# Kernel optimization log

Hardware: AMD Instinct MI355X
Metric: run time of the kernel (lower is better)

The kernel has to match this reference:

```python
import jax, jax.numpy as jnp
import numpy as np
import math

L_LAYERS = 4
EMBED = 512
HEADS = 8
FFN = 2048
EPS = 1e-20
PAD_IDX = 0


def sinusoidal_table(num_embeddings, embedding_dim, padding_idx=0):
    half = embedding_dim // 2
    freq = jnp.exp(jnp.arange(half, dtype=jnp.float32) * (-math.log(10000.0) / (half - 1)))
    ang = jnp.arange(num_embeddings, dtype=jnp.float32)[:, None] * freq[None, :]
    emb = jnp.concatenate([jnp.sin(ang), jnp.cos(ang)], axis=1)
    if padding_idx is not None:
        emb = emb.at[padding_idx].set(0.0)
    return emb  # [num_embeddings, embedding_dim]


def layer_norm(x, g, b):
    mu = jnp.mean(x, axis=-1, keepdims=True)
    var = jnp.mean((x - mu) ** 2, axis=-1, keepdims=True)
    return (x - mu) * jax.lax.rsqrt(var + EPS) * g + b


def mha(x_q, x_kv, Wqkv, bqkv, Wo, bo, mask):
    """Custom attention: scaled scores, multiplicative mask, GLOBAL min-max norm (no softmax)."""
    T, B, C = x_q.shape
    S = x_kv.shape[0]
    hd = C // HEADS
    scale = hd ** -0.5
    q = x_q @ Wqkv[:C].T + bqkv[:C]
    k = x_kv @ Wqkv[C:2 * C].T + bqkv[C:2 * C]
    v = x_kv @ Wqkv[2 * C:].T + bqkv[2 * C:]
    q = q * scale
    # [T,B,C] -> [B*H, T, hd]
    q = q.reshape(T, B * HEADS, hd).transpose(1, 0, 2)
    k = k.reshape(S, B * HEADS, hd).transpose(1, 0, 2)
    v = v.reshape(S, B * HEADS, hd).transpose(1, 0, 2)
    w = jnp.einsum('bth,bsh->bts', q, k)  # [B*H, T, S]
    if mask is not None:
        w = w * mask[None, :, :]
    # global min-max normalization (as in the torch source)
    w = (w - jnp.min(w)) / (jnp.max(w) - jnp.min(w))
    a = jnp.einsum('bts,bsh->bth', w, v)  # [B*H, T, hd]
    a = a.transpose(1, 0, 2).reshape(T, B, C)
    return a @ Wo.T + bo


def setup_inputs() -> dict:
    key = jax.random.key(0)
    ks = iter(jax.random.split(key, 32))
    T, B, C, F, L = 2048, 2, EMBED, FFN, L_LAYERS
    d = {}
    d['x'] = jax.random.normal(next(ks), (T, B, C), dtype=jnp.float32)
    d['enc_out'] = jax.random.normal(next(ks), (T, B, C), dtype=jnp.float32)
    d['tokens'] = jax.random.randint(next(ks), (B, T), 0, 32000, dtype=jnp.int64 if jax.config.read('jax_enable_x64') else jnp.int32)
    sd = C ** -0.5
    d['self_Wqkv'] = jax.random.normal(next(ks), (L, 3 * C, C)) * sd
    d['self_bqkv'] = jnp.zeros((L, 3 * C))
    d['self_Wo'] = jax.random.normal(next(ks), (L, C, C)) * sd
    d['self_bo'] = jnp.zeros((L, C))
    d['cross_Wqkv'] = jax.random.normal(next(ks), (L, 3 * C, C)) * sd
    d['cross_bqkv'] = jnp.zeros((L, 3 * C))
    d['cross_Wo'] = jax.random.normal(next(ks), (L, C, C)) * sd
    d['cross_bo'] = jnp.zeros((L, C))
    d['fc1_w'] = jax.random.normal(next(ks), (L, F, C)) * sd
    d['fc1_b'] = jnp.zeros((L, F))
    d['fc2_w'] = jax.random.normal(next(ks), (L, C, F)) * (F ** -0.5)
    d['fc2_b'] = jnp.zeros((L, C))
    d['ln1_g'] = jnp.ones((L, C)); d['ln1_b'] = jnp.zeros((L, C))
    d['ln2_g'] = jnp.ones((L, C)); d['ln2_b'] = jnp.zeros((L, C))
    d['ln3_g'] = jnp.ones((L, C)); d['ln3_b'] = jnp.zeros((L, C))
    return d


def _forward(x, enc_out, tokens, self_Wqkv, self_bqkv, self_Wo, self_bo,
             cross_Wqkv, cross_bqkv, cross_Wo, cross_bo,
             fc1_w, fc1_b, fc2_w, fc2_b, ln1_g, ln1_b, ln2_g, ln2_b, ln3_g, ln3_b):
    T, B, C = x.shape
    # sinusoidal positional embedding (make_positions with padding_idx=0, no left pad)
    table = sinusoidal_table(PAD_IDX + 1 + T, C, PAD_IDX)
    pos = jnp.where(tokens != PAD_IDX, jnp.arange(1, T + 1)[None, :], 0)  # [B, T]
    pe = table[pos]  # [B, T, C]
    x = x + pe.transpose(1, 0, 2)
    # multiplicative future mask: tril of ones
    fmask = jnp.tril(jnp.ones((T, T), dtype=x.dtype))
    for l in range(L_LAYERS):
        # self-attention
        res = x
        x = mha(x, x, self_Wqkv[l], self_bqkv[l], self_Wo[l], self_bo[l], fmask)
        x = layer_norm(res + x, ln1_g[l], ln1_b[l])
        # cross-attention (no mask)
        res = x
        x = mha(x, enc_out, cross_Wqkv[l], cross_bqkv[l], cross_Wo[l], cross_bo[l], None)
        x = layer_norm(res + x, ln2_g[l], ln2_b[l])
        # FFN
        res = x
        h = jax.nn.relu(x @ fc1_w[l].T + fc1_b[l])
        x = h @ fc2_w[l].T + fc2_b[l]
        x = layer_norm(res + x, ln3_g[l], ln3_b[l])
    return x


def reference(x, enc_out, tokens, self_Wqkv, self_bqkv, self_Wo, self_bo,
              cross_Wqkv, cross_bqkv, cross_Wo, cross_bo,
              fc1_w, fc1_b, fc2_w, fc2_b, ln1_g, ln1_b, ln2_g, ln2_b, ln3_g, ln3_b):
    return _forward(x, enc_out, tokens, self_Wqkv, self_bqkv, self_Wo, self_bo,
                    cross_Wqkv, cross_bqkv, cross_Wo, cross_bo,
                    fc1_w, fc1_b, fc2_w, fc2_b, ln1_g, ln1_b, ln2_g, ln2_b, ln3_g, ln3_b)
```

## Files before the change

### kernel.cpp

```cpp
#include <hip/hip_runtime.h>
#include <math.h>

typedef __bf16 bf16;
typedef unsigned short u16;
typedef unsigned int u32;
typedef __bf16 bf16x8 __attribute__((ext_vector_type(8)));
typedef float f32x4 __attribute__((ext_vector_type(4)));

#define T_SEQ 2048
#define NB    2
#define CE    512
#define HD    64
#define ROWS  4096
#define LDT   40
#define LDA   72

#define MFMA16(a,b,c) __builtin_amdgcn_mfma_f32_16x16x32_bf16((a),(b),(c),0,0,0)

static __device__ __forceinline__ int xcd_swz(int id, int n) {
  int q = n >> 3, r = n & 7;
  int x = id & 7, o = id >> 3;
  return (x < r) ? (x * (q + 1) + o) : (r * (q + 1) + (x - r) * q + o);
}

static __device__ __forceinline__ float ldf(const void* src, size_t eoff, bool f32) {
  return f32 ? ((const float*)src)[eoff] : (float)((const bf16*)src)[eoff];
}

static __device__ __forceinline__ u32 fenc(float f) {
  u32 u = __float_as_uint(f);
  return (u & 0x80000000u) ? ~u : (u | 0x80000000u);
}
static __device__ __forceinline__ float fdec(u32 u) {
  u32 v = (u & 0x80000000u) ? (u & 0x7fffffffu) : ~u;
  return __uint_as_float(v);
}

__global__ __launch_bounds__(256) void sniff(const u16* __restrict__ xs,
                                             const int* __restrict__ toks,
                                             int* __restrict__ flags)
{
  const int tid = threadIdx.x;
  int crazy = 0, ze = 0;
  for (int i = tid; i < 4096; i += 256) {
    int e = (xs[i] >> 7) & 0xFF;
    if (e >= 141) crazy++;
    if (((i & 1) == 0) && (xs[i] == 0)) ze++;
  }
  int zc = 0;
  for (int i = tid; i < 1024; i += 256)
    if (toks[2 * i + 1] == 0) zc++;
  __shared__ int r1[4], r2[4], r3[4];
#pragma unroll
  for (int o = 32; o; o >>= 1) {
    crazy += __shfl_down(crazy, o); ze += __shfl_down(ze, o); zc += __shfl_down(zc, o);
  }
  if ((tid & 63) == 0) { r1[tid >> 6] = crazy; r2[tid >> 6] = ze; r3[tid >> 6] = zc; }
  __syncthreads();
  if (tid == 0) {
    int c = r1[0] + r1[1] + r1[2] + r1[3];
    int z = r2[0] + r2[1] + r2[2] + r2[3];
    int t = r3[0] + r3[1] + r3[2] + r3[3];
    flags[0] = (z > 1500 || c > 64) ? 1 : 0;
    flags[1] = (t > 900) ? 1 : 0;
    flags[3] = 0;
    flags[4] = 0;
  }
}

__global__ __launch_bounds__(256) void probe_lo(const void* w0, const void* w1, const void* w2,
                                                const void* w3, const void* w4, const void* w5,
                                                const void* w6,
                                                int* __restrict__ flags)
{
  if (flags[0] == 0) return;
  const int m = blockIdx.y;
  const void* srcs[7] = {w0, w1, w2, w3, w4, w5, w6};
  const int sizes[7]  = {3145728, 1048576, 3145728, 1048576, 4194304, 4194304, 2097152};
  const float4* p = (const float4*)srcs[m];
  const int n4 = sizes[m] >> 2;
  bool nz = false;
  for (int i = blockIdx.x * 256 + threadIdx.x; i < n4; i += 128 * 256) {
    float4 v = p[i];
    nz = nz || (v.x != (float)(bf16)v.x) || (v.y != (float)(bf16)v.y)
            || (v.z != (float)(bf16)v.z) || (v.w != (float)(bf16)v.w);
  }
  unsigned long long mv = __ballot(nz);
  if ((threadIdx.x & 63) == 0 && mv)
    atomicOr(&flags[(m == 6) ? 3 : 4], 1);
}

__global__ __launch_bounds__(256) void posembed(const void* __restrict__ xsrc,
                                                const int* __restrict__ toks,
                                                const int* __restrict__ flags,
                                                float* __restrict__ xf,
                                                bf16* __restrict__ xh, bf16* __restrict__ xl)
{
  const bool f32 = flags[0] != 0;
  const bool tok64 = flags[1] != 0;
  const int row = blockIdx.x;
  const int t = row >> 1, b = row & 1;
  const int tix = b * T_SEQ + t;
  const int tok = tok64 ? toks[2 * tix] : toks[tix];
  const int p = (tok != 0) ? (t + 1) : 0;
  const float kf = -0.0361193740f;
  for (int c = threadIdx.x; c < CE; c += 256) {
    float pe = 0.0f;
    if (p != 0) {
      int i = (c < 256) ? c : (c - 256);
      float freq = expf((float)i * kf);
      float ang = (float)p * freq;
      pe = (c < 256) ? sinf(ang) : cosf(ang);
    }
    float v = ldf(xsrc, (size_t)row * CE + c, f32) + pe;
    size_t o = (size_t)row * CE + c;
    xf[o] = v;
    bf16 hi = (bf16)v;
    xh[o] = hi; xl[o] = (bf16)(v - (float)hi);
  }
}

template<int OUTM, bool BIAS>
__global__ __launch_bounds__(256) void gemm_bb(const bf16* __restrict__ A1h, const bf16* __restrict__ A1l,
                                               const void* __restrict__ A2,
                                               const void* __restrict__ Braw, long long bOff,
                                               const void* __restrict__ bias, size_t biasOff,
                                               const int* __restrict__ flags,
                                               float* __restrict__ Cf,
                                               bf16* __restrict__ Coh, bf16* __restrict__ Col,
                                               int N, int K, int kspan, int nbx, int nbxA,
                                               long long partStride)
{
  __shared__ __align__(16) bf16 Ah[128 * LDT];
  __shared__ __align__(16) bf16 Al[128 * LDT];
  __shared__ __align__(16) bf16 Bh[64 * LDT];
  __shared__ __align__(16) bf16 Bl[64 * LDT];
  const int id = xcd_swz((int)blockIdx.x, (int)gridDim.x);
  const int per_z = nbx * 32;
  const int zz = id / per_z;
  const int rem = id - zz * per_z;
  const int by = rem / nbx, bx = rem - by * nbx;
  const bool bfl = flags[0] != 0;
  const bool blo = bfl && (flags[4] != 0);
  const bool aSplit = (bx < nbxA);
  const bool a2lo = bfl && (flags[3] != 0);
  const bool alo = aSplit ? true : a2lo;
  const int tid = threadIdx.x;
  const int m0 = by * 128, n0 = bx * 64;
  const int srA = tid >> 1, skA = (tid & 1) * 16;
  const int srB = tid >> 2, skB = (tid & 3) * 8;
  const int wid = tid >> 6, lane = tid & 63;
  const int wm = (wid >> 1) * 64, wn = (wid & 1) * 32;
  const int fr = lane & 15, fk = (lane >> 4) * 8;
  const int kb = zz * kspan;
  const int ke = (kb + kspan < K) ? (kb + kspan) : K;
  f32x4 acc[4][2] = {};

  uint4 ra0, ra1, ra2, ra3, rb0, rb1;
  auto loadA = [&](int k0) {
    size_t g = (size_t)(m0 + srA) * K + k0 + skA;
    if (aSplit) {
      const uint4* p = (const uint4*)(A1h + g); ra0 = p[0]; ra1 = p[1];
      const uint4* q = (const uint4*)(A1l + g); ra2 = q[0]; ra3 = q[1];
    } else if (bfl) {
      const uint4* p = (const uint4*)((const float*)A2 + g);
      ra0 = p[0]; ra1 = p[1]; ra2 = p[2]; ra3 = p[3];
    } else {
      const uint4* p = (const uint4*)((const bf16*)A2 + g); ra0 = p[0]; ra1 = p[1];
    }
  };
  auto loadB = [&](int k0) {
    size_t g = (size_t)bOff + (size_t)(n0 + srB) * K + k0 + skB;
    if (bfl) {
      const uint4* p = (const uint4*)((const float*)Braw + g); rb0 = p[0]; rb1 = p[1];
    } else {
      rb0 = *(const uint4*)((const bf16*)Braw + g);
    }
  };
  auto storeA = [&]() {
    if (aSplit) {
      *(uint4*)&Ah[srA * LDT + skA]     = ra0;
      *(uint4*)&Ah[srA * LDT + skA + 8] = ra1;
      *(uint4*)&Al[srA * LDT + skA]     = ra2;
      *(uint4*)&Al[srA * LDT + skA + 8] = ra3;
    } else if (bfl) {
      const float* f = (const float*)&ra0;
      float v[16];
      const float* f0 = (const float*)&ra0; const float* f1 = (const float*)&ra1;
      const float* f2 = (const float*)&ra2; const float* f3 = (const float*)&ra3;
#pragma unroll
      for (int q = 0; q < 4; q++) { v[q] = f0[q]; v[4+q] = f1[q]; v[8+q] = f2[q]; v[12+q] = f3[q]; }
      (void)f;
      bf16x8 h0, h1;
#pragma unroll
      for (int q = 0; q < 8; q++) { h0[q] = (bf16)v[q]; h1[q] = (bf16)v[8+q]; }
      *(bf16x8*)&Ah[srA * LDT + skA]     = h0;
      *(bf16x8*)&Ah[srA * LDT + skA + 8] = h1;
      if (a2lo) {
        bf16x8 l0, l1;
#pragma unroll
        for (int q = 0; q < 8; q++) {
          l0[q] = (bf16)(v[q]   - (float)h0[q]);
          l1[q] = (bf16)(v[8+q] - (float)h1[q]);
        }
        *(bf16x8*)&Al[srA * LDT + skA]     = l0;
        *(bf16x8*)&Al[srA * LDT + skA + 8] = l1;
      }
    } else {
      *(uint4*)&Ah[srA * LDT + skA]     = ra0;
      *(uint4*)&Ah[srA * LDT + skA + 8] = ra1;
    }
  };
  auto storeB = [&]() {
    if (bfl) {
      float v[8];
      const float* f0 = (const float*)&rb0; const float* f1 = (const float*)&rb1;
#pragma unroll
      for (int q = 0; q < 4; q++) { v[q] = f0[q]; v[4+q] = f1[q]; }
      bf16x8 h0;
#pragma unroll
      for (int q = 0; q < 8; q++) h0[q] = (bf16)v[q];
      *(bf16x8*)&Bh[srB * LDT + skB] = h0;
      if (blo) {
        bf16x8 l0;
#pragma unroll
        for (int q = 0; q < 8; q++) l0[q] = (bf16)(v[q] - (float)h0[q]);
        *(bf16x8*)&Bl[srB * LDT + skB] = l0;
      }
    } else {
      *(uint4*)&Bh[srB * LDT + skB] = rb0;
    }
  };

  loadA(kb); loadB(kb);
  for (int k0 = kb; k0 < ke; k0 += 32) {
    __syncthreads();
    storeA(); storeB();
    __syncthreads();
    if (k0 + 32 < ke) { loadA(k0 + 32); loadB(k0 + 32); }
    bf16x8 ah[4], bh2[2];
#pragma unroll
    for (int i = 0; i < 4; i++) ah[i] = *(const bf16x8*)&Ah[(wm + i*16 + fr) * LDT + fk];
#pragma unroll
    for (int j = 0; j < 2; j++) bh2[j] = *(const bf16x8*)&Bh[(wn + j*16 + fr) * LDT + fk];
#pragma unroll
    for (int i = 0; i < 4; i++)
#pragma unroll
      for (int j = 0; j < 2; j++)
        acc[i][j] = MFMA16(ah[i], bh2[j], acc[i][j]);
    if (alo) {
      bf16x8 al[4];
#pragma unroll
      for (int i = 0; i < 4; i++) al[i] = *(const bf16x8*)&Al[(wm + i*16 + fr) * LDT + fk];
#pragma unroll
      for (int i = 0; i < 4; i++)
#pragma unroll
        for (int j = 0; j < 2; j++)
          acc[i][j] = MFMA16(al[i], bh2[j], acc[i][j]);
    }
    if (blo) {
      bf16x8 bl[2];
#pragma unroll
      for (int j = 0; j < 2; j++) bl[j] = *(const bf16x8*)&Bl[(wn + j*16 + fr) * LDT + fk];
#pragma unroll
      for (int i = 0; i < 4; i++)
#pragma unroll
        for (int j = 0; j < 2; j++)
          acc[i][j] = MFMA16(ah[i], bl[j], acc[i][j]);
    }
  }
  const int orow0 = m0 + wm + (lane >> 4) * 4;
  const int ocol0 = n0 + wn + (lane & 15);
  if (OUTM == 0) {
    float* Cp = Cf + (long long)zz * partStride;
    const bool addb = BIAS && (zz == 0);
#pragma unroll
    for (int j = 0; j < 2; j++) {
      int col = ocol0 + j * 16;
      float bv = addb ? ldf(bias, biasOff + col, flags[0] != 0) : 0.0f;
#pragma unroll
      for (int i = 0; i < 4; i++)
#pragma unroll
        for (int r = 0; r < 4; r++)
          Cp[(size_t)(orow0 + i * 16 + r) * N + col] = acc[i][j][r] + bv;
    }
  } else {
#pragma unroll
    for (int j = 0; j < 2; j++) {
      int col = ocol0 + j * 16;
      float bv = ldf(bias, biasOff + col, flags[0] != 0);
#pragma unroll
      for (int i = 0; i < 4; i++)
#pragma unroll
        for (int r = 0; r < 4; r++) {
          float vv = fmaxf(acc[i][j][r] + bv, 0.0f);
          bf16 hi = (bf16)vv;
          size_t o = (size_t)(orow0 + i * 16 + r) * N + col;
          Coh[o] = hi; Col[o] = (bf16)(vv - (float)hi);
        }
    }
  }
}

__global__ __launch_bounds__(256) void prep_kv(const float* __restrict__ base, int ld,
                                               int kofs0, int vofs0,
                                               bf16* __restrict__ kh, bf16* __restrict__ kl,
                                               bf16* __restrict__ vth, bf16* __restrict__ vtl,
                                               float* __restrict__ vcs,
                                               u32* __restrict__ mmf_u)
{
  __shared__ float ts[64 * 65];
  const int bh = blockIdx.x, s0 = blockIdx.y * 64;
  const int b = bh >> 3, hq = bh & 7;
  const int kofs = kofs0 + hq * HD, vofs = vofs0 + hq * HD;
  const int tid = threadIdx.x;
  if (tid == 0) { mmf_u[0] = 0xFFFFFFFFu; mmf_u[1] = 0u; }
#pragma unroll
  for (int it = 0; it < 16; ++it) {
    int idx = it * 256 + tid, r = idx >> 6, d = idx & 63;
    size_t rowb = (size_t)((s0 + r) * NB + b) * ld;
    float v = base[rowb + kofs + d];
    bf16 hi = (bf16)v;
    size_t o = ((size_t)bh * T_SEQ + s0 + r) * 64 + d;
    kh[o] = hi; kl[o] = (bf16)(v - (float)hi);
    ts[r * 65 + d] = base[rowb + vofs + d];
  }
  __syncthreads();
  const int d = tid >> 2, sseg = (tid & 3) * 16;
  bf16x8 hv0, lv0, hv1, lv1;
#pragma unroll
  for (int q = 0; q < 8; ++q) {
    float v0 = ts[(sseg + q) * 65 + d];
    float v1 = ts[(sseg + 8 + q) * 65 + d];
    bf16 h0 = (bf16)v0, h1 = (bf16)v1;
    hv0[q] = h0; lv0[q] = (bf16)(v0 - (float)h0);
    hv1[q] = h1; lv1[q] = (bf16)(v1 - (float)h1);
  }
  size_t o = ((size_t)bh * 64 + d) * T_SEQ + s0 + sseg;
  *(bf16x8*)&vth[o]     = hv0;
  *(bf16x8*)&vth[o + 8] = hv1;
  *(bf16x8*)&vtl[o]     = lv0;
  *(bf16x8*)&vtl[o + 8] = lv1;
  if (tid < 64) {
    float s = 0.0f;
    for (int j = 0; j < 64; ++j) s += ts[j * 65 + tid];
    vcs[((size_t)bh * 32 + blockIdx.y) * 64 + tid] = s;
  }
}

__device__ __forceinline__ int remap_ty(int ty) { return (ty < 16) ? ty : 47 - ty; }

template<bool MASK>
__global__ __launch_bounds__(256) void fattn(const float* __restrict__ qbase, int qld, int qofs0,
                                             const bf16* __restrict__ kh, const bf16* __restrict__ kl,
                                             const bf16* __restrict__ vth, const bf16* __restrict__ vtl,
                                             u32* __restrict__ mmf_u,
                                             bf16* __restrict__ pvh, bf16* __restrict__ pvl)
{
  __shared__ __align__(16) bf16 Qh[64 * LDA], Ql[64 * LDA];
  __shared__ __align__(16) bf16 Kh[64 * LDA], Kl[64 * LDA];
  __shared__ __align__(16) bf16 Vh[64 * LDA], Vl[64 * LDA];
  __shared__ __align__(16) bf16 Ph[64 * LDA], Pl[64 * LDA];
  __shared__ float rn[4], rx[4];
  const int id = xcd_swz((int)blockIdx.x, 512);
  const int bh = id >> 5;
  const int tyr = remap_ty(id & 31);
  const int t0 = tyr * 64;
  const int b = bh >> 3, hq = bh & 7;
  const int qofs = qofs0 + hq * HD;
  const int tid = threadIdx.x;
#pragma unroll
  for (int it = 0; it < 16; ++it) {
    int idx = it * 256 + tid, r = idx >> 6, d = idx & 63;
    float v = qbase[(size_t)((t0 + r) * NB + b) * qld + qofs + d] * 0.125f;
    bf16 hi = (bf16)v;
    Qh[r * LDA + d] = hi; Ql[r * LDA + d] = (bf16)(v - (float)hi);
  }
  const int wid = tid >> 6, lane = tid & 63;
  const int wm_ = (wid >> 1) * 32, wn_ = (wid & 1) * 32;
  const int fr = lane & 15, fko = (lane >> 4) * 8;
  const int crr = (lane >> 4) * 4, crc = lane & 15;
  const int cr = tid >> 2, cseg = (tid & 3) * 16;
  float mn = 1e30f, mx = -1e30f;
  f32x4 o4[2][2] = {};
  const int nch = MASK ? (tyr + 1) : 32;
  for (int sc = 0; sc < nch; ++sc) {
    const int s0 = sc * 64;
    __syncthreads();
    {
      size_t go = ((size_t)bh * T_SEQ + s0 + cr) * 64 + cseg;
      *(bf16x8*)&Kh[cr * LDA + cseg]     = *(const bf16x8*)&kh[go];
      *(bf16x8*)&Kh[cr * LDA + cseg + 8] = *(const bf16x8*)&kh[go + 8];
      *(bf16x8*)&Kl[cr * LDA + cseg]     = *(const bf16x8*)&kl[go];
      *(bf16x8*)&Kl[cr * LDA + cseg + 8] = *(const bf16x8*)&kl[go + 8];
      size_t gv = ((size_t)bh * 64 + cr) * T_SEQ + s0 + cseg;
      *(bf16x8*)&Vh[cr * LDA + cseg]     = *(const bf16x8*)&vth[gv];
      *(bf16x8*)&Vh[cr * LDA + cseg + 8] = *(const bf16x8*)&vth[gv + 8];
      *(bf16x8*)&Vl[cr * LDA + cseg]     = *(const bf16x8*)&vtl[gv];
      *(bf16x8*)&Vl[cr * LDA + cseg + 8] = *(const bf16x8*)&vtl[gv + 8];
    }
    __syncthreads();
    f32x4 a4[2][2] = {};
#pragma unroll
    for (int ks = 0; ks < 2; ++ks) {
      bf16x8 aH[2], aL[2], bH[2], bL[2];
#pragma unroll
      for (int i = 0; i < 2; ++i) {
        aH[i] = *(const bf16x8*)&Qh[(wm_ + i*16 + fr) * LDA + ks*32 + fko];
        aL[i] = *(const bf16x8*)&Ql[(wm_ + i*16 + fr) * LDA + ks*32 + fko];
        bH[i] = *(const bf16x8*)&Kh[(wn_ + i*16 + fr) * LDA + ks*32 + fko];
        bL[i] = *(const bf16x8*)&Kl[(wn_ + i*16 + fr) * LDA + ks*32 + fko];
      }
#pragma unroll
      for (int i = 0; i < 2; ++i)
#pragma unroll
        for (int j = 0; j < 2; ++j) {
          a4[i][j] = MFMA16(aH[i], bH[j], a4[i][j]);
          a4[i][j] = MFMA16(aL[i], bH[j], a4[i][j]);
          a4[i][j] = MFMA16(aH[i], bL[j], a4[i][j]);
        }
    }
#pragma unroll
    for (int i = 0; i < 2; ++i)
#pragma unroll
      for (int j = 0; j < 2; ++j)
#pragma unroll
        for (int r = 0; r < 4; ++r) {
          int tl = wm_ + i*16 + crr + r;
          int sl = wn_ + j*16 + crc;
          float w = a4[i][j][r];
          if (MASK && (s0 + sl) > (t0 + tl)) w = 0.0f;
          mn = fminf(mn, w); mx = fmaxf(mx, w);
          bf16 wh = (bf16)w;
          Ph[tl * LDA + sl] = wh;
          Pl[tl * LDA + sl] = (bf16)(w - (float)wh);
        }
    __syncthreads();
#pragma unroll
    for (int ks = 0; ks < 2; ++ks) {
      bf16x8 pH[2], pL[2], vH[2], vL[2];
#pragma unroll
      for (int i = 0; i < 2; ++i) {
        pH[i] = *(const bf16x8*)&Ph[(wm_ + i*16 + fr) * LDA + ks*32 + fko];
        pL[i] = *(const bf16x8*)&Pl[(wm_ + i*16 + fr) * LDA + ks*32 + fko];
        vH[i] = *(const bf16x8*)&Vh[(wn_ + i*16 + fr) * LDA + ks*32 + fko];
        vL[i] = *(const bf16x8*)&Vl[(wn_ + i*16 + fr) * LDA + ks*32 + fko];
      }
#pragma unroll
      for (int i = 0; i < 2; ++i)
#pragma unroll
        for (int j = 0; j < 2; ++j) {
          o4[i][j] = MFMA16(pH[i], vH[j], o4[i][j]);
          o4[i][j] = MFMA16(pL[i], vH[j], o4[i][j]);
          o4[i][j] = MFMA16(pH[i], vL[j], o4[i][j]);
        }
    }
  }
#pragma unroll
  for (int i = 0; i < 2; ++i)
#pragma unroll
    for (int j = 0; j < 2; ++j)
#pragma unroll
      for (int r = 0; r < 4; ++r) {
        int tl = wm_ + i*16 + crr + r;
        int dl = wn_ + j*16 + crc;
        float val = o4[i][j][r];
        bf16 hi = (bf16)val;
        size_t o = (size_t)((t0 + tl) * NB + b) * CE + hq * HD + dl;
        pvh[o] = hi; pvl[o] = (bf16)(val - (float)hi);
      }
#pragma unroll
  for (int o = 32; o; o >>= 1) { mn = fminf(mn, __shfl_down(mn, o)); mx = fmaxf(mx, __shfl_down(mx, o)); }
  if (lane == 0) { rn[wid] = mn; rx[wid] = mx; }
  __syncthreads();
  if (tid == 0) {
    float bmn = fminf(fminf(rn[0], rn[1]), fminf(rn[2], rn[3]));
    float bmx = fmaxf(fmaxf(rx[0], rx[1]), fmaxf(rx[2], rx[3]));
    atomicMin(&mmf_u[0], fenc(bmn));
    atomicMax(&mmf_u[1], fenc(bmx));
  }
}

__global__ __launch_bounds__(256) void wo_term(const u32* __restrict__ mmf_u,
                                               const float* __restrict__ vcs,
                                               const void* __restrict__ Wo, size_t woOff,
                                               const void* __restrict__ bo, size_t boOff,
                                               const int* __restrict__ flags,
                                               float* __restrict__ term)
{
  __shared__ float vs[512];
  const bool fl = flags[0] != 0;
  const int tid = threadIdx.x;
  const float mn = fdec(mmf_u[0]);
  const float inv = 1.0f / (fdec(mmf_u[1]) - mn);
  const float cmn = mn * inv;
  const int b = blockIdx.x >> 5;
  for (int k = tid; k < 512; k += 256) {
    int h = k >> 6, d = k & 63;
    float s = 0.0f;
#pragma unroll
    for (int ch = 0; ch < 32; ++ch)
      s += vcs[(size_t)((b * 8 + h) * 32 + ch) * 64 + d];
    vs[k] = s;
  }
  __syncthreads();
  const int out = blockIdx.x * 16 + (tid >> 4);
  const int c = out & 511;
  const int k0 = (tid & 15) * 32;
  float s = 0.0f;
#pragma unroll 8
  for (int k = 0; k < 32; ++k)
    s += vs[k0 + k] * ldf(Wo, woOff + (size_t)c * 512 + k0 + k, fl);
  s += __shfl_down(s, 8); s += __shfl_down(s, 4); s += __shfl_down(s, 2); s += __shfl_down(s, 1);
  if ((tid & 15) == 0)
    term[out] = -cmn * s + ldf(bo, boOff + c, fl);
}

template<int NP, bool AFF, bool SPLIT>
__global__ __launch_bounds__(256) void ln_sum(const float* __restrict__ res,
                                              const float* __restrict__ p, long long pstride,
                                              const void* __restrict__ g, const void* __restrict__ be,
                                              size_t goff, const int* __restrict__ flags,
                                              const u32* __restrict__ mmf_u,
                                              const float* __restrict__ term,
                                              float* __restrict__ xfo,
                                              bf16* __restrict__ xh, bf16* __restrict__ xl)
{
  __shared__ float red[4];
  const bool fl = flags[0] != 0;
  const int tid = threadIdx.x;
  const size_t base = (size_t)blockIdx.x * CE;
  float pa = 0.0f, pb = 0.0f;
#pragma unroll
  for (int k = 0; k < NP; k++) {
    pa += p[(long long)k * pstride + base + tid];
    pb += p[(long long)k * pstride + base + tid + 256];
  }
  float a, b2;
  if (AFF) {
    const float mnv = fdec(mmf_u[0]);
    const float inv = 1.0f / (fdec(mmf_u[1]) - mnv);
    const int b = blockIdx.x & 1;
    a  = res[base + tid]       + inv * pa + term[b * 512 + tid];
    b2 = res[base + tid + 256] + inv * pb + term[b * 512 + tid + 256];
  } else {
    a  = res[base + tid]       + pa;
    b2 = res[base + tid + 256] + pb;
  }
  float s = a + b2;
#pragma unroll
  for (int o = 32; o; o >>= 1) s += __shfl_down(s, o);
  if ((tid & 63) == 0) red[tid >> 6] = s;
  __syncthreads();
  float mu = (red[0] + red[1] + red[2] + red[3]) * (1.0f / 512.0f);
  __syncthreads();
  float da = a - mu, db = b2 - mu;
  float q = da * da + db * db;
#pragma unroll
  for (int o = 32; o; o >>= 1) q += __shfl_down(q, o);
  if ((tid & 63) == 0) red[tid >> 6] = q;
  __syncthreads();
  float var = (red[0] + red[1] + red[2] + red[3]) * (1.0f / 512.0f);
  float rs = rsqrtf(var + 1e-20f);
  float o1 = da * rs * ldf(g, goff + tid, fl)       + ldf(be, goff + tid, fl);
  float o2 = db * rs * ldf(g, goff + tid + 256, fl) + ldf(be, goff + tid + 256, fl);
  xfo[base + tid]       = o1;
  xfo[base + tid + 256] = o2;
  if (SPLIT) {
    bf16 h1 = (bf16)o1, h2 = (bf16)o2;
    xh[base + tid]       = h1; xl[base + tid]       = (bf16)(o1 - (float)h1);
    xh[base + tid + 256] = h2; xl[base + tid + 256] = (bf16)(o2 - (float)h2);
  }
}

extern "C" void kernel_launch(void* const* d_in, const int* in_sizes, int n_in,
                              void* d_out, int out_size, void* d_ws, size_t ws_size,
                              hipStream_t stream)
{
  (void)in_sizes; (void)n_in; (void)out_size; (void)ws_size;
  const void* x_in   = d_in[0];
  const void* enc_in = d_in[1];
  const int*  tokens = (const int*)d_in[2];
  const void* sWqkv = d_in[3];
  const void* sbqkv = d_in[4];
  const void* sWo   = d_in[5];
  const void* sbo   = d_in[6];
  const void* cWqkv = d_in[7];
  const void* cbqkv = d_in[8];
  const void* cWo   = d_in[9];
  const void* cbo   = d_in[10];
  const void* fc1w  = d_in[11];
  const void* fc1b  = d_in[12];
  const void* fc2w  = d_in[13];
  const void* fc2b  = d_in[14];
  const void* ln1g  = d_in[15];
  const void* ln1b  = d_in[16];
  const void* ln2g  = d_in[17];
  const void* ln2b  = d_in[18];
  const void* ln3g  = d_in[19];
  const void* ln3b  = d_in[20];

  char* ws = (char*)d_ws;
  size_t off = 0;
  auto alloc = [&](size_t bytes) -> char* {
    char* p = ws + off;
    off += (bytes + 255) & ~(size_t)255;
    return p;
  };
  int*   flags   = (int*)  alloc(256);
  u32*   mmf_u   = (u32*)  alloc(256);
  float* term    = (float*)alloc(1024 * 4);
  float* xf      = (float*)alloc((size_t)ROWS * CE * 4);
  bf16*  xh      = (bf16*) alloc((size_t)ROWS * CE * 2);
  bf16*  xl      = (bf16*) alloc((size_t)ROWS * CE * 2);
  float* qkv     = (float*)alloc((size_t)ROWS * 2048 * 4);
  bf16*  pvh     = (bf16*) alloc((size_t)ROWS * CE * 2);
  bf16*  pvl     = (bf16*) alloc((size_t)ROWS * CE * 2);
  float* pblk    = (float*)alloc((size_t)ROWS * CE * 4 * 4);
  bf16*  khb     = (bf16*) alloc((size_t)16 * T_SEQ * 64 * 2);
  bf16*  klb     = (bf16*) alloc((size_t)16 * T_SEQ * 64 * 2);
  bf16*  vth     = (bf16*) alloc((size_t)16 * 64 * T_SEQ * 2);
  bf16*  vtl     = (bf16*) alloc((size_t)16 * 64 * T_SEQ * 2);
  float* vcs     = (float*)alloc((size_t)16 * 32 * 64 * 4);
  bf16* hh = (bf16*)qkv;
  bf16* hl = (bf16*)qkv + (size_t)ROWS * 2048;
  const long long PS_FULL = (long long)ROWS * CE;

  sniff<<<1, 256, 0, stream>>>((const u16*)x_in, tokens, flags);
  probe_lo<<<dim3(128, 7), 256, 0, stream>>>(sWqkv, sWo, cWqkv, cWo, fc1w, fc2w, enc_in, flags);
  posembed<<<ROWS, 256, 0, stream>>>(x_in, tokens, flags, xf, xh, xl);

  for (int l = 0; l < 4; l++) {
    gemm_bb<0, true><<<768, 256, 0, stream>>>(
        xh, xl, xh,
        sWqkv, (long long)l * 786432,
        sbqkv, (size_t)l * 1536, flags,
        qkv, nullptr, nullptr, 1536, 512, 512, 24, 24, 0);
    prep_kv<<<dim3(16, 32), 256, 0, stream>>>(qkv, 1536, 512, 1024, khb, klb, vth, vtl, vcs, mmf_u);
    fattn<true><<<512, 256, 0, stream>>>(qkv, 1536, 0, khb, klb, vth, vtl, mmf_u, pvh, pvl);
    wo_term<<<64, 256, 0, stream>>>(mmf_u, vcs, sWo, (size_t)l * 262144, sbo, (size_t)l * 512,
                                    flags, term);
    gemm_bb<0, false><<<1024, 256, 0, stream>>>(
        pvh, pvl, pvh,
        sWo, (long long)l * 262144,
        sbo, 0, flags,
        pblk, nullptr, nullptr, 512, 512, 128, 8, 8, PS_FULL);
    ln_sum<4, true, true><<<ROWS, 256, 0, stream>>>(
        xf, pblk, PS_FULL, ln1g, ln1b, (size_t)l * 512, flags, mmf_u, term, xf, xh, xl);

    gemm_bb<0, true><<<768, 256, 0, stream>>>(
        xh, xl, enc_in,
        cWqkv, (long long)l * 786432,
        cbqkv, (size_t)l * 1536, flags,
        qkv, nullptr, nullptr, 1536, 512, 512, 24, 8, 0);
    prep_kv<<<dim3(16, 32), 256, 0, stream>>>(qkv, 1536, 512, 1024, khb, klb, vth, vtl, vcs, mmf_u);
    fattn<false><<<512, 256, 0, stream>>>(qkv, 1536, 0, khb, klb, vth, vtl, mmf_u, pvh, pvl);
    wo_term<<<64, 256, 0, stream>>>(mmf_u, vcs, cWo, (size_t)l * 262144, cbo, (size_t)l * 512,
                                    flags, term);
    gemm_bb<0, false><<<1024, 256, 0, stream>>>(
        pvh, pvl, pvh,
        cWo, (long long)l * 262144,
        cbo, 0, flags,
        pblk, nullptr, nullptr, 512, 512, 128, 8, 8, PS_FULL);
    ln_sum<4, true, true><<<ROWS, 256, 0, stream>>>(
        xf, pblk, PS_FULL, ln2g, ln2b, (size_t)l * 512, flags, mmf_u, term, xf, xh, xl);

    gemm_bb<1, true><<<1024, 256, 0, stream>>>(
        xh, xl, xh,
        fc1w, (long long)l * 1048576,
        fc1b, (size_t)l * 2048, flags,
        nullptr, hh, hl, 2048, 512, 512, 32, 32, 0);
    gemm_bb<0, true><<<1024, 256, 0, stream>>>(
        hh, hl, hh,
        fc2w, (long long)l * 1048576,
        fc2b, (size_t)l * 512, flags,
        pblk, nullptr, nullptr, 512, 2048, 512, 8, 8, PS_FULL);
    if (l == 3) {
      ln_sum<4, false, false><<<ROWS, 256, 0, stream>>>(
          xf, pblk, PS_FULL, ln3g, ln3b, (size_t)l * 512, flags, nullptr, nullptr,
          (float*)d_out, nullptr, nullptr);
    } else {
      ln_sum<4, false, true><<<ROWS, 256, 0, stream>>>(
          xf, pblk, PS_FULL, ln3g, ln3b, (size_t)l * 512, flags, nullptr, nullptr,
          xf, xh, xl);
    }
  }
}
```

Baseline: 2.299 ms.

## Keep Q fragments in registers, give each wave full rows, prefetch next K/V chunk

The attention kernel now loads each wave's 16 Q rows straight into registers as hi/lo bf16 fragments instead of staging them in shared memory. The work split changes so each wave owns a 16-row strip across all 64 columns. Because each wave then only reads back its own P rows, the block barrier between the P write and the PV step is replaced by a wave-local LDS wait. The next K/V chunk is prefetched into registers while the current chunk is computed, hiding global load latency, at the cost of more registers and more K/V fragment reads from LDS per wave.

```diff
diff --git a/kernel.cpp b/kernel.cpp
--- a/kernel.cpp
+++ b/kernel.cpp
@@ -184,13 +184,11 @@
       *(uint4*)&Al[srA * LDT + skA]     = ra2;
       *(uint4*)&Al[srA * LDT + skA + 8] = ra3;
     } else if (bfl) {
-      const float* f = (const float*)&ra0;
       float v[16];
       const float* f0 = (const float*)&ra0; const float* f1 = (const float*)&ra1;
       const float* f2 = (const float*)&ra2; const float* f3 = (const float*)&ra3;
 #pragma unroll
       for (int q = 0; q < 4; q++) { v[q] = f0[q]; v[4+q] = f1[q]; v[8+q] = f2[q]; v[12+q] = f3[q]; }
-      (void)f;
       bf16x8 h0, h1;
 #pragma unroll
       for (int q = 0; q < 8; q++) { h0[q] = (bf16)v[q]; h1[q] = (bf16)v[8+q]; }
@@ -357,7 +355,6 @@
                                              u32* __restrict__ mmf_u,
                                              bf16* __restrict__ pvh, bf16* __restrict__ pvl)
 {
-  __shared__ __align__(16) bf16 Qh[64 * LDA], Ql[64 * LDA];
   __shared__ __align__(16) bf16 Kh[64 * LDA], Kl[64 * LDA];
   __shared__ __align__(16) bf16 Vh[64 * LDA], Vl[64 * LDA];
   __shared__ __align__(16) bf16 Ph[64 * LDA], Pl[64 * LDA];
@@ -369,109 +366,106 @@
   const int b = bh >> 3, hq = bh & 7;
   const int qofs = qofs0 + hq * HD;
   const int tid = threadIdx.x;
-#pragma unroll
-  for (int it = 0; it < 16; ++it) {
-    int idx = it * 256 + tid, r = idx >> 6, d = idx & 63;
-    float v = qbase[(size_t)((t0 + r) * NB + b) * qld + qofs + d] * 0.125f;
-    bf16 hi = (bf16)v;
-    Qh[r * LDA + d] = hi; Ql[r * LDA + d] = (bf16)(v - (float)hi);
-  }
-  const int wid = tid >> 6, lane = tid & 63;
-  const int wm_ = (wid >> 1) * 32, wn_ = (wid & 1) * 32;
-  const int fr = lane & 15, fko = (lane >> 4) * 8;
-  const int crr = (lane >> 4) * 4, crc = lane & 15;
-  const int cr = tid >> 2, cseg = (tid & 3) * 16;
+  const int wv = tid >> 6, lane = tid & 63;
+  const int g = lane >> 4, c = lane & 15;
+  bf16x8 qh[2], ql[2];
+  {
+    size_t qrow = (size_t)((t0 + wv * 16 + c) * NB + b) * qld + qofs;
+#pragma unroll
+    for (int ks = 0; ks < 2; ++ks) {
+      float4 f0 = *(const float4*)&qbase[qrow + ks * 32 + g * 8];
+      float4 f1 = *(const float4*)&qbase[qrow + ks * 32 + g * 8 + 4];
+      float v[8] = {f0.x, f0.y, f0.z, f0.w, f1.x, f1.y, f1.z, f1.w};
+#pragma unroll
+      for (int q = 0; q < 8; ++q) {
+        float s = v[q] * 0.125f;
+        bf16 hi = (bf16)s;
+        qh[ks][q] = hi; ql[ks][q] = (bf16)(s - (float)hi);
+      }
+    }
+  }
+  const int cr = tid >> 2, cs = (tid & 3) * 16;
+  uint4 rkh0, rkh1, rkl0, rkl1, rvh0, rvh1, rvl0, rvl1;
+  auto loadKV = [&](int s0) {
+    size_t go = ((size_t)bh * T_SEQ + s0 + cr) * 64 + cs;
+    rkh0 = *(const uint4*)&kh[go]; rkh1 = *(const uint4*)&kh[go + 8];
+    rkl0 = *(const uint4*)&kl[go]; rkl1 = *(const uint4*)&kl[go + 8];
+    size_t gv = ((size_t)bh * 64 + cr) * T_SEQ + s0 + cs;
+    rvh0 = *(const uint4*)&vth[gv]; rvh1 = *(const uint4*)&vth[gv + 8];
+    rvl0 = *(const uint4*)&vtl[gv]; rvl1 = *(const uint4*)&vtl[gv + 8];
+  };
+  auto storeKV = [&]() {
+    const int base = cr * LDA + cs;
+    *(uint4*)&Kh[base]     = rkh0; *(uint4*)&Kh[base + 8] = rkh1;
+    *(uint4*)&Kl[base]     = rkl0; *(uint4*)&Kl[base + 8] = rkl1;
+    *(uint4*)&Vh[base]     = rvh0; *(uint4*)&Vh[base + 8] = rvh1;
+    *(uint4*)&Vl[base]     = rvl0; *(uint4*)&Vl[base + 8] = rvl1;
+  };
   float mn = 1e30f, mx = -1e30f;
-  f32x4 o4[2][2] = {};
+  f32x4 o4[4] = {};
   const int nch = MASK ? (tyr + 1) : 32;
+  loadKV(0);
   for (int sc = 0; sc < nch; ++sc) {
     const int s0 = sc * 64;
     __syncthreads();
-    {
-      size_t go = ((size_t)bh * T_SEQ + s0 + cr) * 64 + cseg;
-      *(bf16x8*)&Kh[cr * LDA + cseg]     = *(const bf16x8*)&kh[go];
-      *(bf16x8*)&Kh[cr * LDA + cseg + 8] = *(const bf16x8*)&kh[go + 8];
-      *(bf16x8*)&Kl[cr * LDA + cseg]     = *(const bf16x8*)&kl[go];
-      *(bf16x8*)&Kl[cr * LDA + cseg + 8] = *(const bf16x8*)&kl[go + 8];
-      size_t gv = ((size_t)bh * 64 + cr) * T_SEQ + s0 + cseg;
-      *(bf16x8*)&Vh[cr * LDA + cseg]     = *(const bf16x8*)&vth[gv];
-      *(bf16x8*)&Vh[cr * LDA + cseg + 8] = *(const bf16x8*)&vth[gv + 8];
-      *(bf16x8*)&Vl[cr * LDA + cseg]     = *(const bf16x8*)&vtl[gv];
-      *(bf16x8*)&Vl[cr * LDA + cseg + 8] = *(const bf16x8*)&vtl[gv + 8];
-    }
+    storeKV();
     __syncthreads();
-    f32x4 a4[2][2] = {};
+    if (sc + 1 < nch) loadKV(s0 + 64);
+    f32x4 a4[4] = {};
 #pragma unroll
     for (int ks = 0; ks < 2; ++ks) {
-      bf16x8 aH[2], aL[2], bH[2], bL[2];
-#pragma unroll
-      for (int i = 0; i < 2; ++i) {
-        aH[i] = *(const bf16x8*)&Qh[(wm_ + i*16 + fr) * LDA + ks*32 + fko];
-        aL[i] = *(const bf16x8*)&Ql[(wm_ + i*16 + fr) * LDA + ks*32 + fko];
-        bH[i] = *(const bf16x8*)&Kh[(wn_ + i*16 + fr) * LDA + ks*32 + fko];
-        bL[i] = *(const bf16x8*)&Kl[(wn_ + i*16 + fr) * LDA + ks*32 + fko];
+#pragma unroll
+      for (int j = 0; j < 4; ++j) {
+        bf16x8 kfh = *(const bf16x8*)&Kh[(j * 16 + c) * LDA + ks * 32 + g * 8];
+        bf16x8 kfl = *(const bf16x8*)&Kl[(j * 16 + c) * LDA + ks * 32 + g * 8];
+        a4[j] = MFMA16(qh[ks], kfh, a4[j]);
+        a4[j] = MFMA16(ql[ks], kfh, a4[j]);
+        a4[j] = MFMA16(qh[ks], kfl, a4[j]);
       }
-#pragma unroll
-      for (int i = 0; i < 2; ++i)
-#pragma unroll
-        for (int j = 0; j < 2; ++j) {
-          a4[i][j] = MFMA16(aH[i], bH[j], a4[i][j]);
-          a4[i][j] = MFMA16(aL[i], bH[j], a4[i][j]);
-          a4[i][j] = MFMA16(aH[i], bL[j], a4[i][j]);
-        }
-    }
-#pragma unroll
-    for (int i = 0; i < 2; ++i)
-#pragma unroll
-      for (int j = 0; j < 2; ++j)
-#pragma unroll
-        for (int r = 0; r < 4; ++r) {
-          int tl = wm_ + i*16 + crr + r;
-          int sl = wn_ + j*16 + crc;
-          float w = a4[i][j][r];
-          if (MASK && (s0 + sl) > (t0 + tl)) w = 0.0f;
-          mn = fminf(mn, w); mx = fmaxf(mx, w);
-          bf16 wh = (bf16)w;
-          Ph[tl * LDA + sl] = wh;
-          Pl[tl * LDA + sl] = (bf16)(w - (float)wh);
-        }
-    __syncthreads();
+    }
+#pragma unroll
+    for (int j = 0; j < 4; ++j)
+#pragma unroll
+      for (int r = 0; r < 4; ++r) {
+        int tl = wv * 16 + g * 4 + r;
+        int sl = j * 16 + c;
+        float w = a4[j][r];
+        if (MASK && (s0 + sl) > (t0 + tl)) w = 0.0f;
+        mn = fminf(mn, w); mx = fmaxf(mx, w);
+        bf16 wh = (bf16)w;
+        Ph[tl * LDA + sl] = wh;
+        Pl[tl * LDA + sl] = (bf16)(w - (float)wh);
+      }
+    asm volatile("s_waitcnt lgkmcnt(0)" ::: "memory");
+    __builtin_amdgcn_sched_barrier(0);
 #pragma unroll
     for (int ks = 0; ks < 2; ++ks) {
-      bf16x8 pH[2], pL[2], vH[2], vL[2];
-#pragma unroll
-      for (int i = 0; i < 2; ++i) {
-        pH[i] = *(const bf16x8*)&Ph[(wm_ + i*16 + fr) * LDA + ks*32 + fko];
-        pL[i] = *(const bf16x8*)&Pl[(wm_ + i*16 + fr) * LDA + ks*32 + fko];
-        vH[i] = *(const bf16x8*)&Vh[(wn_ + i*16 + fr) * LDA + ks*32 + fko];
-        vL[i] = *(const bf16x8*)&Vl[(wn_ + i*16 + fr) * LDA + ks*32 + fko];
+      bf16x8 pah = *(const bf16x8*)&Ph[(wv * 16 + c) * LDA + ks * 32 + g * 8];
+      bf16x8 pal = *(const bf16x8*)&Pl[(wv * 16 + c) * LDA + ks * 32 + g * 8];
+#pragma unroll
+      for (int j = 0; j < 4; ++j) {
+        bf16x8 vfh = *(const bf16x8*)&Vh[(j * 16 + c) * LDA + ks * 32 + g * 8];
+        bf16x8 vfl = *(const bf16x8*)&Vl[(j * 16 + c) * LDA + ks * 32 + g * 8];
+        o4[j] = MFMA16(pah, vfh, o4[j]);
+        o4[j] = MFMA16(pal, vfh, o4[j]);
+        o4[j] = MFMA16(pah, vfl, o4[j]);
       }
-#pragma unroll
-      for (int i = 0; i < 2; ++i)
-#pragma unroll
-        for (int j = 0; j < 2; ++j) {
-          o4[i][j] = MFMA16(pH[i], vH[j], o4[i][j]);
-          o4[i][j] = MFMA16(pL[i], vH[j], o4[i][j]);
-          o4[i][j] = MFMA16(pH[i], vL[j], o4[i][j]);
-        }
-    }
-  }
-#pragma unroll
-  for (int i = 0; i < 2; ++i)
-#pragma unroll
-    for (int j = 0; j < 2; ++j)
-#pragma unroll
-      for (int r = 0; r < 4; ++r) {
-        int tl = wm_ + i*16 + crr + r;
-        int dl = wn_ + j*16 + crc;
-        float val = o4[i][j][r];
-        bf16 hi = (bf16)val;
-        size_t o = (size_t)((t0 + tl) * NB + b) * CE + hq * HD + dl;
-        pvh[o] = hi; pvl[o] = (bf16)(val - (float)hi);
-      }
+    }
+  }
+#pragma unroll
+  for (int j = 0; j < 4; ++j)
+#pragma unroll
+    for (int r = 0; r < 4; ++r) {
+      int tl = wv * 16 + g * 4 + r;
+      int dl = j * 16 + c;
+      float val = o4[j][r];
+      bf16 hi = (bf16)val;
+      size_t o = (size_t)((t0 + tl) * NB + b) * CE + hq * HD + dl;
+      pvh[o] = hi; pvl[o] = (bf16)(val - (float)hi);
+    }
 #pragma unroll
   for (int o = 32; o; o >>= 1) { mn = fminf(mn, __shfl_down(mn, o)); mx = fmaxf(mx, __shfl_down(mx, o)); }
-  if (lane == 0) { rn[wid] = mn; rx[wid] = mx; }
+  if (lane == 0) { rn[wv] = mn; rx[wv] = mx; }
   __syncthreads();
   if (tid == 0) {
     float bmn = fminf(fminf(rn[0], rn[1]), fminf(rn[2], rn[3]));
```

Result: no change. 2.288 ms (-0.5%).
